# Optimization experiments

Hardware: AMD Instinct MI355X
Metric: run time of the kernel (lower is better)

Reference implementation:

```python
import jax, jax.numpy as jnp
import numpy as np

D_MODEL = 512
H = 8
D_FF = 2048
EPS = 1e-6
NEG_INF = -1.0e9


def setup_inputs() -> dict:
    key = jax.random.key(0)
    ks = jax.random.split(key, 12)
    B, S, D, F = 8, 2048, D_MODEL, D_FF
    s = 0.02
    inp = {
        "x": jax.random.normal(ks[0], (B, S, D), jnp.float32),
        "src_mask": jnp.ones((B, 1, 1, S), jnp.int32),
        "w_q": jax.random.normal(ks[1], (D, D), jnp.float32) * s,
        "b_q": jnp.zeros((D,), jnp.float32),
        "w_k": jax.random.normal(ks[2], (D, D), jnp.float32) * s,
        "b_k": jnp.zeros((D,), jnp.float32),
        "w_v": jax.random.normal(ks[3], (D, D), jnp.float32) * s,
        "b_v": jnp.zeros((D,), jnp.float32),
        "w_o": jax.random.normal(ks[4], (D, D), jnp.float32) * s,
        "b_o": jnp.zeros((D,), jnp.float32),
        "w_1": jax.random.normal(ks[5], (F, D), jnp.float32) * s,
        "b_1": jnp.zeros((F,), jnp.float32),
        "w_2": jax.random.normal(ks[6], (D, F), jnp.float32) * s,
        "b_2": jnp.zeros((D,), jnp.float32),
    }
    return inp


def _layer_norm(x):
    # Matches torch: (x - mu) / sqrt(std**2 + eps), std is UNBIASED (ddof=1);
    # alpha/bias params exist in the module but are never applied in forward.
    mu = jnp.mean(x, axis=-1, keepdims=True)
    var = jnp.var(x, axis=-1, keepdims=True, ddof=1)
    return (x - mu) / jnp.sqrt(var + EPS)


def _mha(x, src_mask, w_q, b_q, w_k, b_k, w_v, b_v, w_o, b_o):
    B, S, D = x.shape
    d_k = D // H
    q = x @ w_q.T + b_q
    k = x @ w_k.T + b_k
    v = x @ w_v.T + b_v
    # (B, S, H, d_k) -> (B, H, S, d_k)
    q = q.reshape(B, S, H, d_k).transpose(0, 2, 1, 3)
    k = k.reshape(B, S, H, d_k).transpose(0, 2, 1, 3)
    v = v.reshape(B, S, H, d_k).transpose(0, 2, 1, 3)
    scores = jnp.einsum("bhqd,bhkd->bhqk", q, k) / jnp.sqrt(jnp.float32(d_k))
    scores = jnp.where(src_mask == 0, NEG_INF, scores)
    attn = jax.nn.softmax(scores, axis=-1)  # (B, H, S, S) materialized, as in source
    out = jnp.einsum("bhqk,bhkd->bhqd", attn, v)
    out = out.transpose(0, 2, 1, 3).reshape(B, S, D)
    return out @ w_o.T + b_o


def _ffn(x, w_1, b_1, w_2, b_2):
    return jax.nn.relu(x @ w_1.T + b_1) @ w_2.T + b_2


def reference(x, src_mask, w_q, b_q, w_k, b_k, w_v, b_v, w_o, b_o, w_1, b_1, w_2, b_2):
    # dropout prob = 0.0 -> identity (eval-equivalent)
    x1 = x + _mha(_layer_norm(x), src_mask, w_q, b_q, w_k, b_k, w_v, b_v, w_o, b_o)
    return x1 + _ffn(_layer_norm(x1), w_1, b_1, w_2, b_2)
```

## Files before the change

### kernel.cpp

```cpp
#include <hip/hip_runtime.h>
#include <hip/hip_bf16.h>

typedef unsigned short u16;
typedef __bf16 bf16x8 __attribute__((ext_vector_type(8)));
typedef __bf16 bf16x4 __attribute__((ext_vector_type(4)));
typedef unsigned int u32x4 __attribute__((ext_vector_type(4)));
typedef float f32x4 __attribute__((ext_vector_type(4)));

#define SEQ 2048
#define DMODEL 512
#define NHEAD 8
#define DFF 2048
#define NBATCH 8
#define MROWS (NBATCH * SEQ)

#define C1_FOLD 0.18033688f

__device__ __forceinline__ u16 f2b(float f) {
    __hip_bfloat16 h = __float2bfloat16(f);
    u16 u;
    __builtin_memcpy(&u, &h, 2);
    return u;
}

__device__ __forceinline__ unsigned int pack2(float a, float b) {
    float2 f{a, b};
    __hip_bfloat162 h = __float22bfloat162_rn(f);
    unsigned int u;
    __builtin_memcpy(&u, &h, 4);
    return u;
}

__device__ __forceinline__ float ex2(float x) {
#if __has_builtin(__builtin_amdgcn_exp2f)
    return __builtin_amdgcn_exp2f(x);
#else
    return exp2f(x);
#endif
}

__device__ __forceinline__ void gload_lds16(const void* g, void* lds) {
    auto* gp = reinterpret_cast<const __attribute__((address_space(1))) unsigned int*>(
        reinterpret_cast<uintptr_t>(g));
    auto* lp = reinterpret_cast<__attribute__((address_space(3))) unsigned int*>(
        reinterpret_cast<uintptr_t>(lds));
    __builtin_amdgcn_global_load_lds(gp, lp, 16, 0, 0);
}

__global__ __launch_bounds__(256) void cast_weights(
    const float* __restrict__ w0, const float* __restrict__ w1,
    const float* __restrict__ w2, const float* __restrict__ w3,
    const float* __restrict__ w4, const float* __restrict__ w5,
    u16* __restrict__ d0, u16* __restrict__ d1, u16* __restrict__ d2,
    u16* __restrict__ d3, u16* __restrict__ d4, u16* __restrict__ d5) {
    int blk = blockIdx.x;
    const float* s;
    u16* d;
    int base;
    float sc = 1.0f;
    if (blk < 512) {
        int seg = blk >> 7, lb = blk & 127;
        s = seg == 0 ? w0 : seg == 1 ? w1 : seg == 2 ? w2 : w3;
        d = seg == 0 ? d0 : seg == 1 ? d1 : seg == 2 ? d2 : d3;
        base = lb * 2048;
        if (seg == 0) sc = C1_FOLD;
    } else if (blk < 1024) {
        s = w4; d = d4; base = (blk - 512) * 2048;
    } else {
        s = w5; d = d5; base = (blk - 1024) * 2048;
    }
    int i = base + threadIdx.x * 8;
    float4 a = *reinterpret_cast<const float4*>(s + i);
    float4 b = *reinterpret_cast<const float4*>(s + i + 4);
    ushort4 oa, ob;
    oa.x = f2b(a.x * sc); oa.y = f2b(a.y * sc);
    oa.z = f2b(a.z * sc); oa.w = f2b(a.w * sc);
    ob.x = f2b(b.x * sc); ob.y = f2b(b.y * sc);
    ob.z = f2b(b.z * sc); ob.w = f2b(b.w * sc);
    *reinterpret_cast<ushort4*>(d + i) = oa;
    *reinterpret_cast<ushort4*>(d + i + 4) = ob;
}

__global__ __launch_bounds__(256) void concat_bias(const float* __restrict__ bq,
                                                   const float* __restrict__ bk,
                                                   const float* __restrict__ bv,
                                                   float* __restrict__ dst) {
    int i = blockIdx.x * 256 + threadIdx.x;
    float v = i < 512 ? bq[i] * C1_FOLD : (i < 1024 ? bk[i - 512] : bv[i - 1024]);
    dst[i] = v;
}

__global__ __launch_bounds__(256) void ln_rows(const float* __restrict__ x,
                                               u16* __restrict__ out) {
    int row = blockIdx.x * 4 + (threadIdx.x >> 6);
    int l = threadIdx.x & 63;
    const float* xr = x + (size_t)row * DMODEL + l * 8;
    float4 a = *reinterpret_cast<const float4*>(xr);
    float4 b = *reinterpret_cast<const float4*>(xr + 4);
    float s = a.x + a.y + a.z + a.w + b.x + b.y + b.z + b.w;
    float q = a.x * a.x + a.y * a.y + a.z * a.z + a.w * a.w +
              b.x * b.x + b.y * b.y + b.z * b.z + b.w * b.w;
#pragma unroll
    for (int d = 32; d >= 1; d >>= 1) {
        s += __shfl_xor(s, d, 64);
        q += __shfl_xor(q, d, 64);
    }
    float mean = s * (1.f / 512.f);
    float var = (q - 512.f * mean * mean) * (1.f / 511.f);
    float rs = rsqrtf(var + 1e-6f);
    ushort4 o0, o1;
    o0.x = f2b((a.x - mean) * rs); o0.y = f2b((a.y - mean) * rs);
    o0.z = f2b((a.z - mean) * rs); o0.w = f2b((a.w - mean) * rs);
    o1.x = f2b((b.x - mean) * rs); o1.y = f2b((b.y - mean) * rs);
    o1.z = f2b((b.z - mean) * rs); o1.w = f2b((b.w - mean) * rs);
    u16* op = out + (size_t)row * DMODEL + l * 8;
    *reinterpret_cast<ushort4*>(op) = o0;
    *reinterpret_cast<ushort4*>(op + 4) = o1;
}

template <bool RELU, bool RESID, int OUTMODE>
__global__ __launch_bounds__(256, 2) void gemm_nt(
    const u16* __restrict__ A, const u16* __restrict__ W,
    const float* __restrict__ bias, const float* __restrict__ resid,
    void* __restrict__ Cout, void* __restrict__ Cout2, int N, int K) {
    __shared__ u16 Als[128 * 64];
    __shared__ u16 Bls[128 * 64];
    const int tid = threadIdx.x;
    const int l = tid & 63, w = tid >> 6;
    const int m0 = blockIdx.y * 128;
    const int n0 = blockIdx.x * 128;
    const int wr = (w >> 1) * 64, wc = (w & 1) * 64;
    const int lhi = l >> 4, l15 = l & 15, l7 = l & 7;

    f32x4 acc[4][4] = {};

    const int srow = l >> 3;
    const int scol = ((l & 7) * 8) ^ (srow << 3);

    for (int kt = 0; kt < K; kt += 64) {
        __syncthreads();
#pragma unroll
        for (int i = 0; i < 4; ++i) {
            int cc = w * 4 + i;
            int grow = cc * 8 + srow;
            gload_lds16(&A[(size_t)(m0 + grow) * K + kt + scol], &Als[cc * 512]);
            gload_lds16(&W[(size_t)(n0 + grow) * K + kt + scol], &Bls[cc * 512]);
        }
        __syncthreads();
#pragma unroll
        for (int kk = 0; kk < 2; ++kk) {
            const int koff = (kk * 32 + lhi * 8) ^ (l7 << 3);
            bf16x8 af[4], bfr[4];
#pragma unroll
            for (int m = 0; m < 4; ++m)
                af[m] = *reinterpret_cast<const bf16x8*>(
                    &Als[(wr + m * 16 + l15) * 64 + koff]);
#pragma unroll
            for (int n = 0; n < 4; ++n)
                bfr[n] = *reinterpret_cast<const bf16x8*>(
                    &Bls[(wc + n * 16 + l15) * 64 + koff]);
#pragma unroll
            for (int m = 0; m < 4; ++m)
#pragma unroll
                for (int n = 0; n < 4; ++n)
                    acc[m][n] = __builtin_amdgcn_mfma_f32_16x16x32_bf16(
                        af[m], bfr[n], acc[m][n], 0, 0, 0);
        }
    }

    int colg[4];
    float bv[4];
#pragma unroll
    for (int cn = 0; cn < 4; ++cn) {
        colg[cn] = n0 + wc + cn * 16 + l15;
        bv[cn] = bias[colg[cn]];
    }
#pragma unroll
    for (int am = 0; am < 4; ++am) {
        int rowg = m0 + wr + am * 16 + 4 * lhi;
#pragma unroll
        for (int cn = 0; cn < 4; ++cn) {
            float v[4];
#pragma unroll
            for (int r = 0; r < 4; ++r) {
                float t = acc[am][cn][r] + bv[cn];
                if constexpr (RELU) t = fmaxf(t, 0.f);
                if constexpr (RESID)
                    t += resid[(size_t)(rowg + r) * N + colg[cn]];
                v[r] = t;
            }
            if constexpr (OUTMODE == 0) {
                u16* o = (u16*)Cout;
#pragma unroll
                for (int r = 0; r < 4; ++r)
                    o[(size_t)(rowg + r) * N + colg[cn]] = f2b(v[r]);
            } else if constexpr (OUTMODE == 1) {
                float* o = (float*)Cout;
#pragma unroll
                for (int r = 0; r < 4; ++r)
                    o[(size_t)(rowg + r) * N + colg[cn]] = v[r];
            } else {
                if (n0 < 1024) {
                    u16* o = (u16*)Cout;
#pragma unroll
                    for (int r = 0; r < 4; ++r)
                        o[(size_t)(rowg + r) * 1024 + colg[cn]] = f2b(v[r]);
                } else {
                    u16* o = (u16*)Cout2;
                    int bb = rowg >> 11, sloc = rowg & 2047;
                    int dg = colg[cn] - 1024;
                    ushort4 pk;
                    pk.x = f2b(v[0]); pk.y = f2b(v[1]);
                    pk.z = f2b(v[2]); pk.w = f2b(v[3]);
                    *reinterpret_cast<ushort4*>(
                        &o[(size_t)bb * 1048576 + (size_t)(sloc >> 2) * 2048 +
                           dg * 4]) = pk;
                }
            }
        }
    }
}

__global__ __launch_bounds__(256, 4) void attn_fwd(
    const u16* __restrict__ qk, const u16* __restrict__ v4,
    const int* __restrict__ mask, u16* __restrict__ out) {
    __shared__ u16 Kls[2][64 * 64];
    __shared__ u16 Vls[2][64 * 64];
    const int tid = threadIdx.x;
    const int l = tid & 63, w = tid >> 6;
    const int lhi = l >> 4, l15 = l & 15;
    const int lb = (blockIdx.x & 7) * 128 + (blockIdx.x >> 3);
    const int qt = lb & 15, bh = lb >> 4;
    const int b = bh >> 3, h = bh & 7;
    const int q0 = qt * 128 + w * 32;

    const u16* Qb = qk + (size_t)b * SEQ * 1024 + h * 64;
    const u16* Kb = Qb + 512;
    const u16* Vb4 = v4 + (size_t)b * 1048576 + h * 256;
    const int* Mb = mask + b * SEQ;

    const int srow = l >> 3;
    const int scol = ((l & 7) ^ srow) << 3;

    bf16x8 qf[2][2];
#pragma unroll
    for (int g = 0; g < 2; ++g) {
        size_t qa = (size_t)(q0 + g * 16 + l15) * 1024 + lhi * 8;
        qf[g][0] = *reinterpret_cast<const bf16x8*>(&Qb[qa]);
        qf[g][1] = *reinterpret_cast<const bf16x8*>(&Qb[qa + 32]);
    }

    int allone;
    {
        int acc = 1;
#pragma unroll
        for (int i = 0; i < 8; ++i) {
            int4 mm = *reinterpret_cast<const int4*>(&Mb[l * 32 + i * 4]);
            acc &= mm.x & mm.y & mm.z & mm.w;
        }
        allone = __all(acc == 1);
    }

    float lrun[2] = {0.f, 0.f};
    f32x4 oacc[2][4] = {};

    auto stage = [&](int buf, int kv) {
#pragma unroll
        for (int i = 0; i < 2; ++i) {
            int cc = w * 2 + i;
            int row = cc * 8 + srow;
            gload_lds16(&Kb[(size_t)(kv + row) * 1024 + scol], &Kls[buf][cc * 512]);
            gload_lds16(&Vb4[(size_t)((kv >> 2) + cc * 2 + (l >> 5)) * 2048 +
                             (l & 31) * 8],
                        &Vls[buf][cc * 512]);
        }
    };

    const int sw = (l15 & 7) << 3;

    auto tile = [&](int buf, int kv, bool pf, int pbuf, int pkv) {
        if (pf) stage(pbuf, pkv);
        __builtin_amdgcn_sched_barrier(0);

        f32x4 sc[2][4];
        __builtin_amdgcn_s_setprio(1);
#pragma unroll
        for (int ks = 0; ks < 4; ++ks) {
            int krow = ks * 16 + l15;
            bf16x8 ka0 = *reinterpret_cast<const bf16x8*>(
                &Kls[buf][krow * 64 + ((lhi * 8) ^ sw)]);
            bf16x8 ka1 = *reinterpret_cast<const bf16x8*>(
                &Kls[buf][krow * 64 + ((32 + lhi * 8) ^ sw)]);
#pragma unroll
            for (int g = 0; g < 2; ++g) {
                f32x4 z = {};
                z = __builtin_amdgcn_mfma_f32_16x16x32_bf16(ka0, qf[g][0], z, 0, 0, 0);
                z = __builtin_amdgcn_mfma_f32_16x16x32_bf16(ka1, qf[g][1], z, 0, 0, 0);
                sc[g][ks] = z;
            }
        }
        __builtin_amdgcn_s_setprio(0);

        if (!allone) {
            int4 mm[4];
#pragma unroll
            for (int ks = 0; ks < 4; ++ks)
                mm[ks] = *reinterpret_cast<const int4*>(&Mb[kv + ks * 16 + 4 * lhi]);
#pragma unroll
            for (int ks = 0; ks < 4; ++ks) {
                if (mm[ks].x == 0) { sc[0][ks][0] = -3e38f; sc[1][ks][0] = -3e38f; }
                if (mm[ks].y == 0) { sc[0][ks][1] = -3e38f; sc[1][ks][1] = -3e38f; }
                if (mm[ks].z == 0) { sc[0][ks][2] = -3e38f; sc[1][ks][2] = -3e38f; }
                if (mm[ks].w == 0) { sc[0][ks][3] = -3e38f; sc[1][ks][3] = -3e38f; }
            }
        }

        u32x4 pku[2][2];
#pragma unroll
        for (int g = 0; g < 2; ++g) {
            float ps = 0.f;
#pragma unroll
            for (int ks = 0; ks < 4; ++ks) {
                float p0 = ex2(fminf(sc[g][ks][0], 30.f));
                float p1 = ex2(fminf(sc[g][ks][1], 30.f));
                float p2 = ex2(fminf(sc[g][ks][2], 30.f));
                float p3 = ex2(fminf(sc[g][ks][3], 30.f));
                ps += (p0 + p1) + (p2 + p3);
                pku[g][ks >> 1][(ks & 1) * 2 + 0] = pack2(p0, p1);
                pku[g][ks >> 1][(ks & 1) * 2 + 1] = pack2(p2, p3);
            }
            ps += __shfl_xor(ps, 16, 64);
            ps += __shfl_xor(ps, 32, 64);
            lrun[g] += ps;
        }

        __builtin_amdgcn_s_setprio(1);
#pragma unroll
        for (int kp = 0; kp < 2; ++kp) {
#pragma unroll
            for (int dc = 0; dc < 4; ++dc) {
                int dl4 = (dc * 16 + l15) * 4;
                bf16x4 v0 = *reinterpret_cast<const bf16x4*>(
                    &Vls[buf][(kp * 8 + lhi) * 256 + dl4]);
                bf16x4 v1 = *reinterpret_cast<const bf16x4*>(
                    &Vls[buf][(kp * 8 + 4 + lhi) * 256 + dl4]);
                bf16x8 vb8;
                vb8[0] = v0[0]; vb8[1] = v0[1]; vb8[2] = v0[2]; vb8[3] = v0[3];
                vb8[4] = v1[0]; vb8[5] = v1[1]; vb8[6] = v1[2]; vb8[7] = v1[3];
#pragma unroll
                for (int g = 0; g < 2; ++g)
                    oacc[g][dc] = __builtin_amdgcn_mfma_f32_16x16x32_bf16(
                        __builtin_bit_cast(bf16x8, pku[g][kp]), vb8, oacc[g][dc],
                        0, 0, 0);
            }
        }
        __builtin_amdgcn_s_setprio(0);

        asm volatile("s_waitcnt vmcnt(0)" ::: "memory");
        __builtin_amdgcn_s_barrier();
    };

    stage(0, 0);
    asm volatile("s_waitcnt vmcnt(0)" ::: "memory");
    __builtin_amdgcn_s_barrier();

    for (int tt = 0; tt < 16; ++tt) {
        const int base = tt * 128;
        tile(0, base, true, 1, base + 64);
        tile(1, base + 64, tt < 15, 0, base + 128);
    }

#pragma unroll
    for (int g = 0; g < 2; ++g) {
        float inv = 1.f / lrun[g];
        float invr[4];
#pragma unroll
        for (int r = 0; r < 4; ++r) invr[r] = __shfl(inv, 4 * lhi + r, 16);
#pragma unroll
        for (int r = 0; r < 4; ++r) {
            size_t rowa =
                ((size_t)b * SEQ + q0 + g * 16 + 4 * lhi + r) * DMODEL + h * 64;
#pragma unroll
            for (int dc = 0; dc < 4; ++dc)
                out[rowa + dc * 16 + l15] = f2b(oacc[g][dc][r] * invr[r]);
        }
    }
}

extern "C" void kernel_launch(void* const* d_in, const int* in_sizes, int n_in,
                              void* d_out, int out_size, void* d_ws,
                              size_t ws_size, hipStream_t stream) {
    const float* x = (const float*)d_in[0];
    const int* mask = (const int*)d_in[1];
    const float* w_q = (const float*)d_in[2];
    const float* b_q = (const float*)d_in[3];
    const float* w_k = (const float*)d_in[4];
    const float* b_k = (const float*)d_in[5];
    const float* w_v = (const float*)d_in[6];
    const float* b_v = (const float*)d_in[7];
    const float* w_o = (const float*)d_in[8];
    const float* b_o = (const float*)d_in[9];
    const float* w_1 = (const float*)d_in[10];
    const float* b_1 = (const float*)d_in[11];
    const float* w_2 = (const float*)d_in[12];
    const float* b_2 = (const float*)d_in[13];

    char* ws = (char*)d_ws;
    const size_t MB = 1024ull * 1024ull;
    u16* lnx = (u16*)(ws + 0);
    u16* qkb = (u16*)(ws + 16 * MB);
    u16* v4 = (u16*)(ws + 48 * MB);
    u16* lnx1 = (u16*)(ws + 16 * MB);
    u16* hbuf = (u16*)(ws + 32 * MB);
    u16* wqkv = (u16*)(ws + 96 * MB);
    u16* wob = wqkv + 3 * 262144;
    u16* w1b = wqkv + 4 * 262144;
    u16* w2b = w1b + 1048576;
    float* bqkv = (float*)(w2b + 1048576);
    u16* attn_o = lnx;
    float* x1 = (float*)d_out;

    cast_weights<<<1536, 256, 0, stream>>>(
        w_q, w_k, w_v, w_o, w_1, w_2, wqkv, wqkv + 262144, wqkv + 2 * 262144,
        wob, w1b, w2b);
    concat_bias<<<6, 256, 0, stream>>>(b_q, b_k, b_v, bqkv);
    ln_rows<<<4096, 256, 0, stream>>>(x, lnx);

    dim3 g12(12, 128), g4(4, 128), g16(16, 128);
    gemm_nt<false, false, 3><<<g12, 256, 0, stream>>>(lnx, wqkv, bqkv, nullptr,
                                                      qkb, v4, 1536, 512);
    attn_fwd<<<1024, 256, 0, stream>>>(qkb, v4, mask, attn_o);
    gemm_nt<false, true, 1><<<g4, 256, 0, stream>>>(attn_o, wob, b_o, x, x1,
                                                    nullptr, 512, 512);
    ln_rows<<<4096, 256, 0, stream>>>(x1, lnx1);
    gemm_nt<true, false, 0><<<g16, 256, 0, stream>>>(lnx1, w1b, b_1, nullptr,
                                                     hbuf, nullptr, 2048, 512);
    gemm_nt<false, true, 1><<<g4, 256, 0, stream>>>(hbuf, w2b, b_2, x1,
                                                    (float*)d_out, nullptr,
                                                    512, 2048);
}
```

Measured before the change: 290.0 us.

## Double-buffer GEMM LDS tiles to overlap global loads with MFMA compute

The NT GEMM now keeps two LDS buffers for its A and W tiles and issues the direct-to-LDS loads for the next k-tile before computing the current one. Barriers are replaced with explicit vmcnt waits and s_barrier calls, with sched_barrier fences so the compiler keeps the loads ahead of the math. The aim is to hide global memory latency behind the matrix instructions, at the cost of doubling GEMM shared memory (64 KB per block), which can limit how many blocks fit per CU. Separately, the attention kernel's launch bound is lowered from 4 to 3 blocks per SM, which gives the compiler more registers per thread but may reduce occupancy.

```diff
diff --git a/kernel.cpp b/kernel.cpp
--- a/kernel.cpp
+++ b/kernel.cpp
@@ -123,8 +123,8 @@
     const u16* __restrict__ A, const u16* __restrict__ W,
     const float* __restrict__ bias, const float* __restrict__ resid,
     void* __restrict__ Cout, void* __restrict__ Cout2, int N, int K) {
-    __shared__ u16 Als[128 * 64];
-    __shared__ u16 Bls[128 * 64];
+    __shared__ u16 Als[2][128 * 64];
+    __shared__ u16 Bls[2][128 * 64];
     const int tid = threadIdx.x;
     const int l = tid & 63, w = tid >> 6;
     const int m0 = blockIdx.y * 128;
@@ -137,16 +137,19 @@
     const int srow = l >> 3;
     const int scol = ((l & 7) * 8) ^ (srow << 3);
 
-    for (int kt = 0; kt < K; kt += 64) {
-        __syncthreads();
+    auto stage = [&](int buf, int kt) {
 #pragma unroll
         for (int i = 0; i < 4; ++i) {
             int cc = w * 4 + i;
             int grow = cc * 8 + srow;
-            gload_lds16(&A[(size_t)(m0 + grow) * K + kt + scol], &Als[cc * 512]);
-            gload_lds16(&W[(size_t)(n0 + grow) * K + kt + scol], &Bls[cc * 512]);
-        }
-        __syncthreads();
+            gload_lds16(&A[(size_t)(m0 + grow) * K + kt + scol],
+                        &Als[buf][cc * 512]);
+            gload_lds16(&W[(size_t)(n0 + grow) * K + kt + scol],
+                        &Bls[buf][cc * 512]);
+        }
+    };
+
+    auto compute = [&](int buf) {
 #pragma unroll
         for (int kk = 0; kk < 2; ++kk) {
             const int koff = (kk * 32 + lhi * 8) ^ (l7 << 3);
@@ -154,11 +157,11 @@
 #pragma unroll
             for (int m = 0; m < 4; ++m)
                 af[m] = *reinterpret_cast<const bf16x8*>(
-                    &Als[(wr + m * 16 + l15) * 64 + koff]);
+                    &Als[buf][(wr + m * 16 + l15) * 64 + koff]);
 #pragma unroll
             for (int n = 0; n < 4; ++n)
                 bfr[n] = *reinterpret_cast<const bf16x8*>(
-                    &Bls[(wc + n * 16 + l15) * 64 + koff]);
+                    &Bls[buf][(wc + n * 16 + l15) * 64 + koff]);
 #pragma unroll
             for (int m = 0; m < 4; ++m)
 #pragma unroll
@@ -166,6 +169,23 @@
                     acc[m][n] = __builtin_amdgcn_mfma_f32_16x16x32_bf16(
                         af[m], bfr[n], acc[m][n], 0, 0, 0);
         }
+    };
+
+    stage(0, 0);
+    asm volatile("s_waitcnt vmcnt(0)" ::: "memory");
+    __builtin_amdgcn_s_barrier();
+
+    for (int kt = 0; kt < K; kt += 128) {
+        if (kt + 64 < K) stage(1, kt + 64);
+        __builtin_amdgcn_sched_barrier(0);
+        compute(0);
+        asm volatile("s_waitcnt vmcnt(0)" ::: "memory");
+        __builtin_amdgcn_s_barrier();
+        if (kt + 128 < K) stage(0, kt + 128);
+        __builtin_amdgcn_sched_barrier(0);
+        compute(1);
+        asm volatile("s_waitcnt vmcnt(0)" ::: "memory");
+        __builtin_amdgcn_s_barrier();
     }
 
     int colg[4];
@@ -221,7 +241,7 @@
     }
 }
 
-__global__ __launch_bounds__(256, 4) void attn_fwd(
+__global__ __launch_bounds__(256, 3) void attn_fwd(
     const u16* __restrict__ qk, const u16* __restrict__ v4,
     const int* __restrict__ mask, u16* __restrict__ out) {
     __shared__ u16 Kls[2][64 * 64];
```

Measured after the change: 282.5 us. 1.03x faster.
